# Optimization experiments

Measured on AMD Instinct MI355X. Metric: run time of the kernel, lower is better.

The kernel has to match this reference:

```python
import jax, jax.numpy as jnp
import numpy as np

H = 256   # input_size
P = 256   # state_size
BATCH, L = 8, 4096
DT_MIN, DT_MAX = 1e-3, 1e-1
LN_EPS = 1e-5


def _hippo_params():
    # HiPPO-N matrix (num_blocks=1), eigendecomposition in numpy (float64 then cast)
    idx = np.arange(P, dtype=np.float64)
    s = np.sqrt(idx + 0.5)
    A = -np.outer(s, s)
    A = np.tril(A) - np.triu(A, 1)
    np.fill_diagonal(A, -0.5)
    ev, V = np.linalg.eig(A)
    order = np.argsort(ev.real)
    ev, V = ev[order], V[:, order]
    return ev, V


def setup_inputs() -> dict:
    key = jax.random.key(0)
    k_u, = jax.random.split(key, 1)
    ev, V = _hippo_params()
    rng = np.random.default_rng(0)
    log_lambda_real = np.log(-np.clip(ev.real, None, -1e-4)).astype(np.float32)
    lambda_imag = ev.imag.astype(np.float32)
    V_inv = np.linalg.inv(V)
    B_init = rng.standard_normal((P, H)) / np.sqrt(P)
    B_tilde = V_inv @ B_init.astype(np.complex128)
    C_init = rng.standard_normal((H, P)) / np.sqrt(P)
    C_tilde = C_init.astype(np.complex128) @ V
    log_delta = (rng.random(P) * (np.log(DT_MAX) - np.log(DT_MIN)) + np.log(DT_MIN)).astype(np.float32)
    return {
        "u": jax.random.normal(k_u, (BATCH, L, H), dtype=jnp.float32),
        "log_lambda_real": jnp.asarray(log_lambda_real),
        "lambda_imag": jnp.asarray(lambda_imag),
        "B_tilde_real": jnp.asarray(B_tilde.real, dtype=jnp.float32),
        "B_tilde_imag": jnp.asarray(B_tilde.imag, dtype=jnp.float32),
        "C_tilde_real": jnp.asarray(C_tilde.real, dtype=jnp.float32),
        "C_tilde_imag": jnp.asarray(C_tilde.imag, dtype=jnp.float32),
        "log_delta": jnp.asarray(log_delta),
        "gamma": jnp.ones((H,), dtype=jnp.float32),
        "beta": jnp.zeros((H,), dtype=jnp.float32),
    }


def _layernorm(x, gamma, beta):
    mu = jnp.mean(x, axis=-1, keepdims=True)
    var = jnp.mean(jnp.square(x - mu), axis=-1, keepdims=True)
    return (x - mu) * jax.lax.rsqrt(var + LN_EPS) * gamma + beta


def _ssm(h, log_lambda_real, lambda_imag, B_tilde_real, B_tilde_imag,
         C_tilde_real, C_tilde_imag, log_delta):
    # Continuous-time diagonal SSM params
    lam = -jnp.exp(log_lambda_real) + 1j * lambda_imag            # (P,) complex
    B_tilde = B_tilde_real + 1j * B_tilde_imag                     # (P,H)
    C_tilde = C_tilde_real + 1j * C_tilde_imag                     # (H,P)
    delta = jnp.exp(log_delta)                                     # (P,)
    # ZOH discretization (eq. 6 of the S5 paper)
    lambda_bar = jnp.exp(lam * delta)                              # (P,)
    B_bar = ((lambda_bar - 1.0) / lam)[:, None] * B_tilde          # (P,H)
    # Bu_k = B_bar @ u_k  ->  (B,L,P) complex
    Bu = jnp.einsum('blh,ph->blp', h.astype(jnp.complex64), B_bar.astype(jnp.complex64))
    # Parallel associative scan for x_k = lambda_bar * x_{k-1} + Bu_k
    a = jnp.broadcast_to(lambda_bar.astype(jnp.complex64), Bu.shape)
    def combine(c1, c2):
        a1, b1 = c1
        a2, b2 = c2
        return a1 * a2, a2 * b1 + b2
    _, xs = jax.lax.associative_scan(combine, (a, Bu), axis=1)     # (B,L,P)
    # Project back to real output: y = Re(C_tilde @ x)
    y = jnp.einsum('blp,hp->blh', xs, C_tilde.astype(jnp.complex64)).real
    return y


def reference(u, log_lambda_real, lambda_imag, B_tilde_real, B_tilde_imag,
              C_tilde_real, C_tilde_imag, log_delta, gamma, beta):
    # S5Block: pre-LayerNorm -> S5 SSM -> GELU -> residual
    h = _layernorm(u, gamma, beta)
    y = _ssm(h, log_lambda_real, lambda_imag, B_tilde_real, B_tilde_imag,
             C_tilde_real, C_tilde_imag, log_delta)
    return u + jax.nn.gelu(y)
```

## Files before the change

kernel.cpp:

```cpp
#include <hip/hip_runtime.h>
#include <math.h>

#define HDIM 256
#define PDIM 256
#define BATCH 8
#define LSEQ 4096
#define MTOT (BATCH * LSEQ)
#define NCHUNK 128
#define CHLEN 32

typedef __attribute__((ext_vector_type(8))) short bf16x8;
typedef __attribute__((ext_vector_type(4))) float f32x4;

__device__ __forceinline__ unsigned short f2bf(float f) {
    union { float f; unsigned int u; } v; v.f = f;
    unsigned int r = v.u + 0x7FFFu + ((v.u >> 16) & 1u);
    return (unsigned short)(r >> 16);
}
__device__ __forceinline__ float bf2f(unsigned int lo16) {
    union { unsigned int u; float f; } v; v.u = lo16 << 16;
    return v.f;
}

__device__ __forceinline__ void gload_lds16(const void* g, void* l) {
    __builtin_amdgcn_global_load_lds(
        (const __attribute__((address_space(1))) void*)g,
        (__attribute__((address_space(3))) void*)l, 16, 0, 0);
}

__global__ void wpack_k(const float* __restrict__ llr, const float* __restrict__ lim,
                        const float* __restrict__ ldl,
                        const float* __restrict__ Br, const float* __restrict__ Bi,
                        const float* __restrict__ Cr, const float* __restrict__ Ci,
                        unsigned short* __restrict__ W1t, unsigned short* __restrict__ W2t,
                        float* __restrict__ par) {
    int h = threadIdx.x;
    if (blockIdx.x < PDIM) {
        int p = blockIdx.x;
        float er = expf(llr[p]);
        float im = lim[p];
        float d  = expf(ldl[p]);
        float zr = -er * d, zi = im * d;
        float ea = expf(zr);
        float sz, cz; sincosf(zi, &sz, &cz);
        float ar = ea * cz, ai = ea * sz;
        float dr = -er, di = im;
        float den = dr * dr + di * di;
        float nr = ar - 1.0f, ni = ai;
        float cr = (nr * dr + ni * di) / den;
        float ci = (ni * dr - nr * di) / den;
        float br = Br[p * HDIM + h], bi = Bi[p * HDIM + h];
        W1t[(2 * p) * HDIM + h]     = f2bf(cr * br - ci * bi);
        W1t[(2 * p + 1) * HDIM + h] = f2bf(cr * bi + ci * br);
    } else if (blockIdx.x < 2 * PDIM) {
        int p = blockIdx.x - PDIM;
        W2t[h * (2 * PDIM) + 2 * p]     = f2bf(Cr[h * PDIM + p]);
        W2t[h * (2 * PDIM) + 2 * p + 1] = f2bf(-Ci[h * PDIM + p]);
    } else {
        int p = h;
        float er = expf(llr[p]);
        float im = lim[p];
        float d  = expf(ldl[p]);
        float zr = -er * d, zi = im * d;
        float ea = expf(zr);
        float sz, cz; sincosf(zi, &sz, &cz);
        float ar = ea * cz, ai = ea * sz;
        float dr = -er, di = im;
        float den = dr * dr + di * di;
        float nr = ar - 1.0f, ni = ai;
        float cr = (nr * dr + ni * di) / den;
        float ci = (ni * dr - nr * di) / den;
        float eC = expf((float)CHLEN * zr);
        float sC, cC;
        sincosf((float)CHLEN * zi, &sC, &cC);
        par[2 * p]            = ar;
        par[2 * p + 1]        = ai;
        par[512 + 2 * p]      = cr;
        par[512 + 2 * p + 1]  = ci;
        par[1024 + 2 * p]     = eC * cC;
        par[1024 + 2 * p + 1] = eC * sC;
    }
}

__global__ void ln_k(const float* __restrict__ u, unsigned short* __restrict__ hbf,
                     const float* __restrict__ gamma, const float* __restrict__ beta) {
    __shared__ float gS[HDIM], bS[HDIM];
    int t = threadIdx.x;
    gS[t] = gamma[t]; bS[t] = beta[t];
    int lane = t & 63, wv = t >> 6;
    int row = blockIdx.x * 4 + wv;
    float4 v = *(const float4*)(u + (size_t)row * HDIM + lane * 4);
    float s  = v.x + v.y + v.z + v.w;
    float sq = v.x * v.x + v.y * v.y + v.z * v.z + v.w * v.w;
    #pragma unroll
    for (int o = 1; o < 64; o <<= 1) { s += __shfl_xor(s, o); sq += __shfl_xor(sq, o); }
    float mu = s * (1.0f / HDIM);
    float rs = rsqrtf(sq * (1.0f / HDIM) - mu * mu + 1e-5f);
    __syncthreads();
    int c = lane * 4;
    ushort4 o;
    o.x = f2bf((v.x - mu) * rs * gS[c + 0] + bS[c + 0]);
    o.y = f2bf((v.y - mu) * rs * gS[c + 1] + bS[c + 1]);
    o.z = f2bf((v.z - mu) * rs * gS[c + 2] + bS[c + 2]);
    o.w = f2bf((v.w - mu) * rs * gS[c + 3] + bS[c + 3]);
    *(ushort4*)(hbf + (size_t)row * HDIM + c) = o;
}

template <int MODE, int K>
__launch_bounds__(256, 2)
__global__ void mfma_gemm_k(const unsigned short* __restrict__ A,
                            const unsigned short* __restrict__ B,
                            void* __restrict__ outv,
                            const float* __restrict__ u,
                            int N) {
    __shared__ __align__(16) unsigned short As[2][128 * 32];
    __shared__ __align__(16) unsigned short Bs[2][128 * 32];
    const int t = threadIdx.x;

    const int nbn  = (int)gridDim.x;
    const int flat = (int)blockIdx.y * nbn + (int)blockIdx.x;
    const int nwg  = nbn * (int)gridDim.y;
    const int tile = (flat & 7) * (nwg >> 3) + (flat >> 3);
    const int bn = tile % nbn, bm = tile / nbn;

    const int lane = t & 63, w = t >> 6;

    const int srow   = 32 * w + (lane >> 2);
    const int schunk = (lane & 3) ^ ((lane >> 3) & 3);
    const unsigned short* gA = A + (size_t)(bm * 128 + srow) * K + schunk * 8;
    const unsigned short* gB = B + (size_t)(bn * 128 + srow) * K + schunk * 8;
    const int l0 = (32 * w) * 32;
    const int l1 = (32 * w + 16) * 32;

    const int wm = (w & 1) * 64;
    const int wn = (w >> 1) * 64;
    const int mrow = lane & 15;
    const int rsw  = (mrow >> 1) & 3;
    const int cch  = lane >> 4;
    const int fcol = ((cch ^ rsw) * 8);

    f32x4 acc[4][4] = {};
    constexpr int NT = K / 32;

    gload_lds16(gA,          &As[0][l0]);
    gload_lds16(gA + 16 * K, &As[0][l1]);
    gload_lds16(gB,          &Bs[0][l0]);
    gload_lds16(gB + 16 * K, &Bs[0][l1]);

    #pragma unroll
    for (int tt = 0; tt < NT; ++tt) {
        const int cur = tt & 1;
        if (tt + 1 < NT) {
            const int k0 = (tt + 1) * 32;
            gload_lds16(gA + k0,          &As[cur ^ 1][l0]);
            gload_lds16(gA + 16 * K + k0, &As[cur ^ 1][l1]);
            gload_lds16(gB + k0,          &Bs[cur ^ 1][l0]);
            gload_lds16(gB + 16 * K + k0, &Bs[cur ^ 1][l1]);
            asm volatile("s_waitcnt vmcnt(4)" ::: "memory");
        } else {
            asm volatile("s_waitcnt vmcnt(0)" ::: "memory");
        }
        __builtin_amdgcn_sched_barrier(0);
        __builtin_amdgcn_s_barrier();
        __builtin_amdgcn_sched_barrier(0);

        bf16x8 fa[4], fb[4];
        #pragma unroll
        for (int i = 0; i < 4; i++) {
            fa[i] = *(const bf16x8*)&As[cur][(wm + i * 16 + mrow) * 32 + fcol];
            fb[i] = *(const bf16x8*)&Bs[cur][(wn + i * 16 + mrow) * 32 + fcol];
        }
        __builtin_amdgcn_s_setprio(1);
        #pragma unroll
        for (int i = 0; i < 4; i++)
            #pragma unroll
            for (int j = 0; j < 4; j++)
                acc[i][j] = __builtin_amdgcn_mfma_f32_16x16x32_bf16(fa[i], fb[j], acc[i][j], 0, 0, 0);
        __builtin_amdgcn_s_setprio(0);
        __builtin_amdgcn_sched_barrier(0);
        if (tt + 1 < NT) __builtin_amdgcn_s_barrier();
    }

    const int r0 = (lane >> 4) * 4;
    const int c0 = lane & 15;
    #pragma unroll
    for (int i = 0; i < 4; i++) {
        #pragma unroll
        for (int r = 0; r < 4; r++) {
            const size_t rowoff = (size_t)(bm * 128 + wm + i * 16 + r0 + r) * N;
            #pragma unroll
            for (int j = 0; j < 4; j++) {
                const int col_g = bn * 128 + wn + j * 16 + c0;
                float y = acc[i][j][r];
                if (MODE == 0) {
                    ((unsigned short*)outv)[rowoff + col_g] = f2bf(y);
                } else {
                    float z = 0.7978845608f * fmaf(0.044715f * y * y, y, y);
                    float e = __expf(2.0f * z);
                    float th = 1.0f - 2.0f / (e + 1.0f);
                    float g = 0.5f * y * (1.0f + th);
                    ((float*)outv)[rowoff + col_g] = u[rowoff + col_g] + g;
                }
            }
        }
    }
}

__global__ void scan_reduce_k(const unsigned short* __restrict__ Bu,
                              const float* __restrict__ par, float* __restrict__ last) {
    int t = threadIdx.x;
    int lane = t & 63, g = t >> 6;
    int c = blockIdx.x * 4 + g, b = blockIdx.y;
    int p0 = lane * 4;
    float4 a01 = *(const float4*)(par + 2 * p0);
    float4 a23 = *(const float4*)(par + 2 * p0 + 4);
    float ar[4] = {a01.x, a01.z, a23.x, a23.z};
    float ai[4] = {a01.y, a01.w, a23.y, a23.w};
    float xr[4] = {0.f, 0.f, 0.f, 0.f}, xi[4] = {0.f, 0.f, 0.f, 0.f};
    const uint4* q = (const uint4*)(Bu + ((size_t)b * LSEQ + (size_t)c * CHLEN) * 512) + lane;
    #pragma unroll 8
    for (int j = 0; j < CHLEN; j++) {
        uint4 v = q[(size_t)j * 64];
        unsigned int vv[4] = {v.x, v.y, v.z, v.w};
        #pragma unroll
        for (int k = 0; k < 4; k++) {
            float vr = bf2f(vv[k] & 0xFFFFu), vi = bf2f(vv[k] >> 16);
            float nr = fmaf(ar[k], xr[k], fmaf(-ai[k], xi[k], vr));
            float ni = fmaf(ar[k], xi[k], fmaf(ai[k], xr[k], vi));
            xr[k] = nr; xi[k] = ni;
        }
    }
    float* lp = last + ((size_t)b * NCHUNK + c) * 512 + 2 * p0;
    *(float4*)lp       = make_float4(xr[0], xi[0], xr[1], xi[1]);
    *(float4*)(lp + 4) = make_float4(xr[2], xi[2], xr[3], xi[3]);
}

__global__ void scan_carry_k(const float* __restrict__ last, float* __restrict__ prefix,
                             const float* __restrict__ par) {
    int p = threadIdx.x, b = blockIdx.x;
    float Ar = par[1024 + 2 * p], Ai = par[1024 + 2 * p + 1];
    float Pr = 0.0f, Pi = 0.0f;
    const float2* lp = (const float2*)(last + (size_t)b * NCHUNK * 512) + p;
    float2* pp = (float2*)(prefix + (size_t)b * NCHUNK * 512) + p;
    for (int c0 = 0; c0 < NCHUNK; c0 += 16) {
        float2 v[16];
        #pragma unroll
        for (int j = 0; j < 16; j++) v[j] = lp[(size_t)(c0 + j) * 256];
        #pragma unroll
        for (int j = 0; j < 16; j++) {
            pp[(size_t)(c0 + j) * 256] = make_float2(Pr, Pi);
            float nr = fmaf(Ar, Pr, fmaf(-Ai, Pi, v[j].x));
            float ni = fmaf(Ar, Pi, fmaf(Ai, Pr, v[j].y));
            Pr = nr; Pi = ni;
        }
    }
}

__launch_bounds__(256, 2)
__global__ void apply_gemm2_k(const unsigned short* __restrict__ Bu,
                              const float* __restrict__ par,
                              const float* __restrict__ prefix,
                              const unsigned short* __restrict__ W2t,
                              const float* __restrict__ u, float* __restrict__ out) {
    __shared__ __align__(16) unsigned short Xs[32 * 512];
    __shared__ __align__(16) unsigned short Bs[2][256 * 32];
    const int t = threadIdx.x;
    const int lane = t & 63, w = t >> 6;
    const int c = blockIdx.x, b = blockIdx.y;
    const size_t row0 = (size_t)b * LSEQ + (size_t)c * CHLEN;

    const int schunk = (lane & 3) ^ ((lane >> 3) & 3);
    const unsigned short* gW = W2t + (size_t)(w * 64 + (lane >> 2)) * 512 + schunk * 8;

    #pragma unroll
    for (int m = 0; m < 4; m++)
        gload_lds16(gW + (size_t)m * 16 * 512, &Bs[0][(w * 64 + m * 16) * 32]);

    {
        const unsigned int* q = (const unsigned int*)(Bu + row0 * 512) + t;
        unsigned int vv[32];
        #pragma unroll
        for (int j = 0; j < 32; j++) vv[j] = q[(size_t)j * 256];
        const float2 P = ((const float2*)(prefix + ((size_t)b * NCHUNK + c) * 512))[t];
        const float ar = par[2 * t], ai = par[2 * t + 1];
        float xr = P.x, xi = P.y;
        #pragma unroll
        for (int j = 0; j < 32; j++) {
            float vr = bf2f(vv[j] & 0xFFFFu), vi = bf2f(vv[j] >> 16);
            float nr = fmaf(ar, xr, fmaf(-ai, xi, vr));
            float ni = fmaf(ar, xi, fmaf(ai, xr, vi));
            xr = nr; xi = ni;
            unsigned int pk = (unsigned int)f2bf(xr) | ((unsigned int)f2bf(xi) << 16);
            *(unsigned int*)&Xs[j * 512 + ((((t >> 2) ^ (j & 7)) << 3) + (t & 3) * 2)] = pk;
        }
    }

    const int mrow = lane & 15;
    const int rsw  = (mrow >> 1) & 3;
    const int cch  = lane >> 4;
    const int fcol = (cch ^ rsw) * 8;

    f32x4 acc[2][4] = {};
    __syncthreads();

    #pragma unroll
    for (int tt = 0; tt < 16; tt++) {
        const int cur = tt & 1;
        if (tt + 1 < 16) {
            const int k0 = (tt + 1) * 32;
            #pragma unroll
            for (int m = 0; m < 4; m++)
                gload_lds16(gW + (size_t)m * 16 * 512 + k0,
                            &Bs[cur ^ 1][(w * 64 + m * 16) * 32]);
            asm volatile("s_waitcnt vmcnt(4)" ::: "memory");
        } else {
            asm volatile("s_waitcnt vmcnt(0)" ::: "memory");
        }
        __builtin_amdgcn_sched_barrier(0);

        bf16x8 fa[2], fb[4];
        #pragma unroll
        for (int i = 0; i < 2; i++) {
            const int r = i * 16 + mrow;
            fa[i] = *(const bf16x8*)&Xs[r * 512 + (((tt * 4 + cch) ^ (r & 7)) << 3)];
        }
        #pragma unroll
        for (int j = 0; j < 4; j++)
            fb[j] = *(const bf16x8*)&Bs[cur][(w * 64 + j * 16 + mrow) * 32 + fcol];
        __builtin_amdgcn_s_setprio(1);
        #pragma unroll
        for (int i = 0; i < 2; i++)
            #pragma unroll
            for (int j = 0; j < 4; j++)
                acc[i][j] = __builtin_amdgcn_mfma_f32_16x16x32_bf16(fa[i], fb[j], acc[i][j], 0, 0, 0);
        __builtin_amdgcn_s_setprio(0);
        __builtin_amdgcn_sched_barrier(0);
    }

    const int r0 = (lane >> 4) * 4, c0 = lane & 15;
    #pragma unroll
    for (int i = 0; i < 2; i++) {
        #pragma unroll
        for (int r = 0; r < 4; r++) {
            const size_t rowoff = (row0 + i * 16 + r0 + r) * HDIM;
            #pragma unroll
            for (int j = 0; j < 4; j++) {
                const int col = w * 64 + j * 16 + c0;
                float y = acc[i][j][r];
                float z = 0.7978845608f * fmaf(0.044715f * y * y, y, y);
                float e = __expf(2.0f * z);
                float th = 1.0f - 2.0f / (e + 1.0f);
                float g = 0.5f * y * (1.0f + th);
                out[rowoff + col] = u[rowoff + col] + g;
            }
        }
    }
}

extern "C" void kernel_launch(void* const* d_in, const int* in_sizes, int n_in,
                              void* d_out, int out_size, void* d_ws, size_t ws_size,
                              hipStream_t stream) {
    const float* u   = (const float*)d_in[0];
    const float* llr = (const float*)d_in[1];
    const float* lim = (const float*)d_in[2];
    const float* Br  = (const float*)d_in[3];
    const float* Bi  = (const float*)d_in[4];
    const float* Cr  = (const float*)d_in[5];
    const float* Ci  = (const float*)d_in[6];
    const float* ldl = (const float*)d_in[7];
    const float* gam = (const float*)d_in[8];
    const float* bet = (const float*)d_in[9];
    float* out = (float*)d_out;

    float* ws     = (float*)d_ws;
    float* par    = ws;
    float* last   = ws + 2048;
    float* prefix = last + (size_t)BATCH * NCHUNK * 512;
    unsigned short* W1t = (unsigned short*)(prefix + (size_t)BATCH * NCHUNK * 512);
    unsigned short* W2t = W1t + 512 * HDIM;
    unsigned short* hbf = W2t + HDIM * 512;
    unsigned short* Bu  = hbf + (size_t)MTOT * HDIM;

    ln_k<<<MTOT / 4, 256, 0, stream>>>(u, hbf, gam, bet);
    wpack_k<<<2 * PDIM + 1, HDIM, 0, stream>>>(llr, lim, ldl, Br, Bi, Cr, Ci, W1t, W2t, par);

    mfma_gemm_k<0, HDIM><<<dim3(512 / 128, MTOT / 128), 256, 0, stream>>>(
        hbf, W1t, (void*)Bu, nullptr, 512);

    scan_reduce_k<<<dim3(NCHUNK / 4, BATCH), 256, 0, stream>>>(Bu, par, last);
    scan_carry_k<<<BATCH, PDIM, 0, stream>>>(last, prefix, par);

    apply_gemm2_k<<<dim3(NCHUNK, BATCH), 256, 0, stream>>>(Bu, par, prefix, W2t, u, out);
}
```

Before: 163.2 us.

## Replace 4-wave 128x128 GEMM1 tile with single-wave 64x64 tiles without barriers

New measurement: 167.5 us. 2.7% more time.

```diff
diff --git a/kernel.cpp b/kernel.cpp
--- a/kernel.cpp
+++ b/kernel.cpp
@@ -106,16 +106,13 @@
     *(ushort4*)(hbf + (size_t)row * HDIM + c) = o;
 }
 
-template <int MODE, int K>
-__launch_bounds__(256, 2)
-__global__ void mfma_gemm_k(const unsigned short* __restrict__ A,
-                            const unsigned short* __restrict__ B,
-                            void* __restrict__ outv,
-                            const float* __restrict__ u,
-                            int N) {
-    __shared__ __align__(16) unsigned short As[2][128 * 32];
-    __shared__ __align__(16) unsigned short Bs[2][128 * 32];
-    const int t = threadIdx.x;
+__launch_bounds__(64, 4)
+__global__ void gemm1_k(const unsigned short* __restrict__ A,
+                        const unsigned short* __restrict__ W1t,
+                        unsigned short* __restrict__ Bu) {
+    __shared__ __align__(16) unsigned short As[2][64 * 32];
+    __shared__ __align__(16) unsigned short Bs[2][64 * 32];
+    const int lane = threadIdx.x;
 
     const int nbn  = (int)gridDim.x;
     const int flat = (int)blockIdx.y * nbn + (int)blockIdx.x;
@@ -123,52 +120,43 @@
     const int tile = (flat & 7) * (nwg >> 3) + (flat >> 3);
     const int bn = tile % nbn, bm = tile / nbn;
 
-    const int lane = t & 63, w = t >> 6;
-
-    const int srow   = 32 * w + (lane >> 2);
     const int schunk = (lane & 3) ^ ((lane >> 3) & 3);
-    const unsigned short* gA = A + (size_t)(bm * 128 + srow) * K + schunk * 8;
-    const unsigned short* gB = B + (size_t)(bn * 128 + srow) * K + schunk * 8;
-    const int l0 = (32 * w) * 32;
-    const int l1 = (32 * w + 16) * 32;
-
-    const int wm = (w & 1) * 64;
-    const int wn = (w >> 1) * 64;
-    const int mrow = lane & 15;
+    const unsigned short* gA = A   + (size_t)(bm * 64 + (lane >> 2)) * HDIM + schunk * 8;
+    const unsigned short* gB = W1t + (size_t)(bn * 64 + (lane >> 2)) * HDIM + schunk * 8;
+
+    const int mrow = lane & 15, cch = lane >> 4;
     const int rsw  = (mrow >> 1) & 3;
-    const int cch  = lane >> 4;
-    const int fcol = ((cch ^ rsw) * 8);
+    const int fcol = (cch ^ rsw) * 8;
 
     f32x4 acc[4][4] = {};
-    constexpr int NT = K / 32;
-
-    gload_lds16(gA,          &As[0][l0]);
-    gload_lds16(gA + 16 * K, &As[0][l1]);
-    gload_lds16(gB,          &Bs[0][l0]);
-    gload_lds16(gB + 16 * K, &Bs[0][l1]);
-
-    #pragma unroll
-    for (int tt = 0; tt < NT; ++tt) {
+
+    #pragma unroll
+    for (int m = 0; m < 4; m++) {
+        gload_lds16(gA + (size_t)m * 16 * HDIM, &As[0][m * 16 * 32]);
+        gload_lds16(gB + (size_t)m * 16 * HDIM, &Bs[0][m * 16 * 32]);
+    }
+
+    #pragma unroll
+    for (int tt = 0; tt < HDIM / 32; ++tt) {
         const int cur = tt & 1;
-        if (tt + 1 < NT) {
+        if (tt + 1 < HDIM / 32) {
             const int k0 = (tt + 1) * 32;
-            gload_lds16(gA + k0,          &As[cur ^ 1][l0]);
-            gload_lds16(gA + 16 * K + k0, &As[cur ^ 1][l1]);
-            gload_lds16(gB + k0,          &Bs[cur ^ 1][l0]);
-            gload_lds16(gB + 16 * K + k0, &Bs[cur ^ 1][l1]);
-            asm volatile("s_waitcnt vmcnt(4)" ::: "memory");
+            #pragma unroll
+            for (int m = 0; m < 4; m++) {
+                gload_lds16(gA + (size_t)m * 16 * HDIM + k0, &As[cur ^ 1][m * 16 * 32]);
+                gload_lds16(gB + (size_t)m * 16 * HDIM + k0, &Bs[cur ^ 1][m * 16 * 32]);
+            }
+            asm volatile("s_waitcnt vmcnt(8)" ::: "memory");
         } else {
             asm volatile("s_waitcnt vmcnt(0)" ::: "memory");
         }
         __builtin_amdgcn_sched_barrier(0);
-        __builtin_amdgcn_s_barrier();
-        __builtin_amdgcn_sched_barrier(0);
 
         bf16x8 fa[4], fb[4];
         #pragma unroll
         for (int i = 0; i < 4; i++) {
-            fa[i] = *(const bf16x8*)&As[cur][(wm + i * 16 + mrow) * 32 + fcol];
-            fb[i] = *(const bf16x8*)&Bs[cur][(wn + i * 16 + mrow) * 32 + fcol];
+            fa[i] = *(const bf16x8*)&As[cur][(i * 16 + mrow) * 32 + fcol];
+            fb[i] = *(const bf16x8*)&Bs[cur][(i * 16 + mrow) * 32 + fcol];
         }
         __builtin_amdgcn_s_setprio(1);
         #pragma unroll
@@ -178,30 +166,17 @@
                 acc[i][j] = __builtin_amdgcn_mfma_f32_16x16x32_bf16(fa[i], fb[j], acc[i][j], 0, 0, 0);
         __builtin_amdgcn_s_setprio(0);
         __builtin_amdgcn_sched_barrier(0);
-        if (tt + 1 < NT) __builtin_amdgcn_s_barrier();
-    }
-
-    const int r0 = (lane >> 4) * 4;
-    const int c0 = lane & 15;
+    }
+
+    const int r0 = (lane >> 4) * 4, c0 = lane & 15;
     #pragma unroll
     for (int i = 0; i < 4; i++) {
         #pragma unroll
         for (int r = 0; r < 4; r++) {
-            const size_t rowoff = (size_t)(bm * 128 + wm + i * 16 + r0 + r) * N;
-            #pragma unroll
-            for (int j = 0; j < 4; j++) {
-                const int col_g = bn * 128 + wn + j * 16 + c0;
-                float y = acc[i][j][r];
-                if (MODE == 0) {
-                    ((unsigned short*)outv)[rowoff + col_g] = f2bf(y);
-                } else {
-                    float z = 0.7978845608f * fmaf(0.044715f * y * y, y, y);
-                    float e = __expf(2.0f * z);
-                    float th = 1.0f - 2.0f / (e + 1.0f);
-                    float g = 0.5f * y * (1.0f + th);
-                    ((float*)outv)[rowoff + col_g] = u[rowoff + col_g] + g;
-                }
-            }
+            const size_t rowoff = (size_t)(bm * 64 + i * 16 + r0 + r) * 512;
+            #pragma unroll
+            for (int j = 0; j < 4; j++)
+                Bu[rowoff + bn * 64 + j * 16 + c0] = f2bf(acc[i][j][r]);
         }
     }
 }
@@ -384,8 +359,7 @@
     ln_k<<<MTOT / 4, 256, 0, stream>>>(u, hbf, gam, bet);
     wpack_k<<<2 * PDIM + 1, HDIM, 0, stream>>>(llr, lim, ldl, Br, Bi, Cr, Ci, W1t, W2t, par);
 
-    mfma_gemm_k<0, HDIM><<<dim3(512 / 128, MTOT / 128), 256, 0, stream>>>(
-        hbf, W1t, (void*)Bu, nullptr, 512);
+    gemm1_k<<<dim3(8, MTOT / 64), 64, 0, stream>>>(hbf, W1t, Bu);
 
     scan_reduce_k<<<dim3(NCHUNK / 4, BATCH), 256, 0, stream>>>(Bu, par, last);
     scan_carry_k<<<BATCH, PDIM, 0, stream>>>(last, prefix, par);
```

## Fuse chunk scan reduction into first GEMM epilogue via LDS staging

Applied to the files above, without the earlier changes.

After: 155.6 us. 4.6% less time.

```diff
diff --git a/kernel.cpp b/kernel.cpp
--- a/kernel.cpp
+++ b/kernel.cpp
@@ -106,16 +106,20 @@
     *(ushort4*)(hbf + (size_t)row * HDIM + c) = o;
 }
 
-template <int MODE, int K>
 __launch_bounds__(256, 2)
-__global__ void mfma_gemm_k(const unsigned short* __restrict__ A,
-                            const unsigned short* __restrict__ B,
-                            void* __restrict__ outv,
-                            const float* __restrict__ u,
-                            int N) {
-    __shared__ __align__(16) unsigned short As[2][128 * 32];
-    __shared__ __align__(16) unsigned short Bs[2][128 * 32];
+__global__ void gemm1_reduce_k(const unsigned short* __restrict__ A,
+                               const unsigned short* __restrict__ B,
+                               unsigned short* __restrict__ Bu,
+                               const float* __restrict__ par,
+                               float* __restrict__ last) {
+    __shared__ __align__(16) unsigned char smem[128 * 66 * 4];
+    unsigned short* As0 = (unsigned short*)smem;
+    unsigned short* Bs0 = (unsigned short*)(smem + 16384);
+    unsigned int*   Cs  = (unsigned int*)smem;
     const int t = threadIdx.x;
+
+    constexpr int K = HDIM;
+    constexpr int N = 512;
 
     const int nbn  = (int)gridDim.x;
     const int flat = (int)blockIdx.y * nbn + (int)blockIdx.x;
@@ -142,20 +146,20 @@
     f32x4 acc[4][4] = {};
     constexpr int NT = K / 32;
 
-    gload_lds16(gA,          &As[0][l0]);
-    gload_lds16(gA + 16 * K, &As[0][l1]);
-    gload_lds16(gB,          &Bs[0][l0]);
-    gload_lds16(gB + 16 * K, &Bs[0][l1]);
+    gload_lds16(gA,          &As0[0 * 4096 + l0]);
+    gload_lds16(gA + 16 * K, &As0[0 * 4096 + l1]);
+    gload_lds16(gB,          &Bs0[0 * 4096 + l0]);
+    gload_lds16(gB + 16 * K, &Bs0[0 * 4096 + l1]);
 
     #pragma unroll
     for (int tt = 0; tt < NT; ++tt) {
         const int cur = tt & 1;
         if (tt + 1 < NT) {
             const int k0 = (tt + 1) * 32;
-            gload_lds16(gA + k0,          &As[cur ^ 1][l0]);
-            gload_lds16(gA + 16 * K + k0, &As[cur ^ 1][l1]);
-            gload_lds16(gB + k0,          &Bs[cur ^ 1][l0]);
-            gload_lds16(gB + 16 * K + k0, &Bs[cur ^ 1][l1]);
+            gload_lds16(gA + k0,          &As0[(cur ^ 1) * 4096 + l0]);
+            gload_lds16(gA + 16 * K + k0, &As0[(cur ^ 1) * 4096 + l1]);
+            gload_lds16(gB + k0,          &Bs0[(cur ^ 1) * 4096 + l0]);
+            gload_lds16(gB + 16 * K + k0, &Bs0[(cur ^ 1) * 4096 + l1]);
             asm volatile("s_waitcnt vmcnt(4)" ::: "memory");
         } else {
             asm volatile("s_waitcnt vmcnt(0)" ::: "memory");
@@ -167,8 +171,8 @@
         bf16x8 fa[4], fb[4];
         #pragma unroll
         for (int i = 0; i < 4; i++) {
-            fa[i] = *(const bf16x8*)&As[cur][(wm + i * 16 + mrow) * 32 + fcol];
-            fb[i] = *(const bf16x8*)&Bs[cur][(wn + i * 16 + mrow) * 32 + fcol];
+            fa[i] = *(const bf16x8*)&As0[cur * 4096 + (wm + i * 16 + mrow) * 32 + fcol];
+            fb[i] = *(const bf16x8*)&Bs0[cur * 4096 + (wn + i * 16 + mrow) * 32 + fcol];
         }
         __builtin_amdgcn_s_setprio(1);
         #pragma unroll
@@ -181,58 +185,44 @@
         if (tt + 1 < NT) __builtin_amdgcn_s_barrier();
     }
 
+    __syncthreads();
+
+    unsigned short* CsUS = (unsigned short*)Cs;
     const int r0 = (lane >> 4) * 4;
     const int c0 = lane & 15;
     #pragma unroll
     for (int i = 0; i < 4; i++) {
         #pragma unroll
         for (int r = 0; r < 4; r++) {
-            const size_t rowoff = (size_t)(bm * 128 + wm + i * 16 + r0 + r) * N;
+            const int row_l = wm + i * 16 + r0 + r;
+            const size_t rowoff = (size_t)(bm * 128 + row_l) * N;
             #pragma unroll
             for (int j = 0; j < 4; j++) {
-                const int col_g = bn * 128 + wn + j * 16 + c0;
-                float y = acc[i][j][r];
-                if (MODE == 0) {
-                    ((unsigned short*)outv)[rowoff + col_g] = f2bf(y);
-                } else {
-                    float z = 0.7978845608f * fmaf(0.044715f * y * y, y, y);
-                    float e = __expf(2.0f * z);
-                    float th = 1.0f - 2.0f / (e + 1.0f);
-                    float g = 0.5f * y * (1.0f + th);
-                    ((float*)outv)[rowoff + col_g] = u[rowoff + col_g] + g;
-                }
+                const int col_l = wn + j * 16 + c0;
+                const unsigned short hv = f2bf(acc[i][j][r]);
+                Bu[rowoff + bn * 128 + col_l] = hv;
+                CsUS[row_l * 132 + col_l]     = hv;
             }
         }
     }
-}
-
-__global__ void scan_reduce_k(const unsigned short* __restrict__ Bu,
-                              const float* __restrict__ par, float* __restrict__ last) {
-    int t = threadIdx.x;
-    int lane = t & 63, g = t >> 6;
-    int c = blockIdx.x * 4 + g, b = blockIdx.y;
-    int p0 = lane * 4;
-    float4 a01 = *(const float4*)(par + 2 * p0);
-    float4 a23 = *(const float4*)(par + 2 * p0 + 4);
-    float ar[4] = {a01.x, a01.z, a23.x, a23.z};
-    float ai[4] = {a01.y, a01.w, a23.y, a23.w};
-    float xr[4] = {0.f, 0.f, 0.f, 0.f}, xi[4] = {0.f, 0.f, 0.f, 0.f};
-    const uint4* q = (const uint4*)(Bu + ((size_t)b * LSEQ + (size_t)c * CHLEN) * 512) + lane;
+    __syncthreads();
+
+    const int g  = w;
+    const int pg = bn * 64 + lane;
+    const float ar = par[2 * pg], ai = par[2 * pg + 1];
+    float xr = 0.0f, xi = 0.0f;
+    const unsigned int* crow = Cs + (size_t)(g * 32) * 66 + lane;
     #pragma unroll 8
     for (int j = 0; j < CHLEN; j++) {
-        uint4 v = q[(size_t)j * 64];
-        unsigned int vv[4] = {v.x, v.y, v.z, v.w};
-        #pragma unroll
-        for (int k = 0; k < 4; k++) {
-            float vr = bf2f(vv[k] & 0xFFFFu), vi = bf2f(vv[k] >> 16);
-            float nr = fmaf(ar[k], xr[k], fmaf(-ai[k], xi[k], vr));
-            float ni = fmaf(ar[k], xi[k], fmaf(ai[k], xr[k], vi));
-            xr[k] = nr; xi[k] = ni;
-        }
-    }
-    float* lp = last + ((size_t)b * NCHUNK + c) * 512 + 2 * p0;
-    *(float4*)lp       = make_float4(xr[0], xi[0], xr[1], xi[1]);
-    *(float4*)(lp + 4) = make_float4(xr[2], xi[2], xr[3], xi[3]);
+        unsigned int v = crow[(size_t)j * 66];
+        float vr = bf2f(v & 0xFFFFu), vi = bf2f(v >> 16);
+        float nr = fmaf(ar, xr, fmaf(-ai, xi, vr));
+        float ni = fmaf(ar, xi, fmaf(ai, xr, vi));
+        xr = nr; xi = ni;
+    }
+    const int b  = (bm * 128) / LSEQ;
+    const int cg = ((bm * 128) % LSEQ) / CHLEN + g;
+    *(float2*)(last + ((size_t)b * NCHUNK + cg) * 512 + 2 * pg) = make_float2(xr, xi);
 }
 
 __global__ void scan_carry_k(const float* __restrict__ last, float* __restrict__ prefix,
@@ -384,10 +374,8 @@
     ln_k<<<MTOT / 4, 256, 0, stream>>>(u, hbf, gam, bet);
     wpack_k<<<2 * PDIM + 1, HDIM, 0, stream>>>(llr, lim, ldl, Br, Bi, Cr, Ci, W1t, W2t, par);
 
-    mfma_gemm_k<0, HDIM><<<dim3(512 / 128, MTOT / 128), 256, 0, stream>>>(
-        hbf, W1t, (void*)Bu, nullptr, 512);
-
-    scan_reduce_k<<<dim3(NCHUNK / 4, BATCH), 256, 0, stream>>>(Bu, par, last);
+    gemm1_reduce_k<<<dim3(512 / 128, MTOT / 128), 256, 0, stream>>>(hbf, W1t, Bu, par, last);
+
     scan_carry_k<<<BATCH, PDIM, 0, stream>>>(last, prefix, par);
 
     apply_gemm2_k<<<dim3(NCHUNK, BATCH), 256, 0, stream>>>(Bu, par, prefix, W2t, u, out);
```
